# Optimization experiments

Measured on AMD Instinct MI355X. Metric: run time of the kernel, lower is better.

## Reference

```python
import jax, jax.numpy as jnp
import numpy as np

B, S, D_IN, D_OUT, H = 4, 2048, 1024, 1024, 16
HD = D_OUT // H  # head_dim = 64


def setup_inputs() -> dict:
    key = jax.random.key(0)
    ks = jax.random.split(key, 7)
    sd_in = 1.0 / np.sqrt(D_IN)
    sd_out = 1.0 / np.sqrt(D_OUT)
    return {
        "x": jax.random.normal(ks[0], (B, S, D_IN), dtype=jnp.float32),
        # weights stored [in, out] so y = x @ W (equivalent to torch Linear)
        "wq": jax.random.uniform(ks[1], (D_IN, D_OUT), jnp.float32, -sd_in, sd_in),
        "wk": jax.random.uniform(ks[2], (D_IN, D_OUT), jnp.float32, -sd_in, sd_in),
        "wv": jax.random.uniform(ks[3], (D_IN, D_OUT), jnp.float32, -sd_in, sd_in),
        "wo": jax.random.uniform(ks[4], (D_OUT, D_OUT), jnp.float32, -sd_out, sd_out),
        "bo": jax.random.uniform(ks[5], (D_OUT,), jnp.float32, -sd_out, sd_out),
    }


def reference(x, wq, wk, wv, wo, bo):
    b, n, _ = x.shape
    # project and split heads: [b, h, n, hd]
    q = (x @ wq).reshape(b, n, H, HD).transpose(0, 2, 1, 3)
    k = (x @ wk).reshape(b, n, H, HD).transpose(0, 2, 1, 3)
    v = (x @ wv).reshape(b, n, H, HD).transpose(0, 2, 1, 3)
    scale = 1.0 / jnp.sqrt(jnp.asarray(HD, dtype=x.dtype))
    scores = jnp.einsum('bhqd,bhkd->bhqk', q, k) * scale  # [b,h,n,n]
    causal = jnp.tril(jnp.ones((n, n), dtype=bool))
    scores = jnp.where(causal, scores, -jnp.inf)
    attn = jax.nn.softmax(scores, axis=-1)
    # dropout p=0.0 -> identity
    ctx = jnp.einsum('bhqk,bhkd->bhqd', attn, v)
    ctx = ctx.transpose(0, 2, 1, 3).reshape(b, n, D_OUT)
    return ctx @ wo + bo
```

## Files before the change

kernel.cpp:

```cpp
#include <hip/hip_runtime.h>

#define DEVINL __device__ __forceinline__

typedef __attribute__((ext_vector_type(8))) short s8v;
typedef __attribute__((ext_vector_type(4))) float f4v;
typedef __attribute__((ext_vector_type(16))) float f16v;
typedef __attribute__((ext_vector_type(8))) __bf16 bf8v;
typedef __attribute__((ext_vector_type(4))) unsigned int u4v;

static constexpr int SEQ = 2048;
static constexpr int DIM = 1024;
static constexpr int NH = 16;

DEVINL unsigned short f2bf(float f) {
  unsigned int u = __builtin_bit_cast(unsigned int, f);
  u += 0x7FFFu + ((u >> 16) & 1u);
  return (unsigned short)(u >> 16);
}

DEVINL void gl_lds16(const void* g, void* l) {
  __builtin_amdgcn_global_load_lds((__attribute__((address_space(1))) void*)g,
                                   (__attribute__((address_space(3))) void*)l,
                                   16, 0, 0);
}

DEVINL f4v mfma16(s8v a, s8v b, f4v c) {
  return __builtin_amdgcn_mfma_f32_16x16x32_bf16(__builtin_bit_cast(bf8v, a),
                                                 __builtin_bit_cast(bf8v, b),
                                                 c, 0, 0, 0);
}

DEVINL f16v mfma32(s8v a, s8v b, f16v c) {
  return __builtin_amdgcn_mfma_f32_32x32x16_bf16(__builtin_bit_cast(bf8v, a),
                                                 __builtin_bit_cast(bf8v, b),
                                                 c, 0, 0, 0);
}

DEVINL unsigned cvtpk(float lo, float hi) {
  unsigned r;
  asm("v_cvt_pk_bf16_f32 %0, %1, %2" : "=v"(r) : "v"(lo), "v"(hi));
  return r;
}

DEVINL void plswap(unsigned& a, unsigned& b) {
#if __has_builtin(__builtin_amdgcn_permlane32_swap)
  typedef int i2v __attribute__((ext_vector_type(2)));
  i2v r = __builtin_amdgcn_permlane32_swap((int)a, (int)b, false, false);
  a = (unsigned)r[0]; b = (unsigned)r[1];
#else
  asm volatile("v_permlane32_swap_b32 %0, %1" : "+v"(a), "+v"(b));
#endif
}

DEVINL s8v mkfrag(unsigned w0, unsigned w1, unsigned w2, unsigned w3) {
  u4v t = {w0, w1, w2, w3};
  return __builtin_bit_cast(s8v, t);
}

__global__ __launch_bounds__(256) void k_cvt(const float* __restrict__ in,
                                             unsigned short* __restrict__ outp) {
  const int i = blockIdx.x * 256 + threadIdx.x;
  const f4v* p = (const f4v*)in + (size_t)i * 2;
  f4v a = p[0], b = p[1];
  s8v o;
  o[0] = (short)f2bf(a[0]); o[1] = (short)f2bf(a[1]);
  o[2] = (short)f2bf(a[2]); o[3] = (short)f2bf(a[3]);
  o[4] = (short)f2bf(b[0]); o[5] = (short)f2bf(b[1]);
  o[6] = (short)f2bf(b[2]); o[7] = (short)f2bf(b[3]);
  ((s8v*)outp)[i] = o;
}

__global__ __launch_bounds__(256) void k_twt(const float* __restrict__ w0, const float* __restrict__ w1,
                                             const float* __restrict__ w2, const float* __restrict__ w3,
                                             unsigned short* __restrict__ o0, unsigned short* __restrict__ o1,
                                             unsigned short* __restrict__ o2, unsigned short* __restrict__ o3) {
  __shared__ float tile[32][33];
  const float* w = blockIdx.z == 0 ? w0 : blockIdx.z == 1 ? w1 : blockIdx.z == 2 ? w2 : w3;
  unsigned short* o = blockIdx.z == 0 ? o0 : blockIdx.z == 1 ? o1 : blockIdx.z == 2 ? o2 : o3;
  const int r0 = blockIdx.y * 32, c0 = blockIdx.x * 32;
  const int tx = threadIdx.x & 31, ty = threadIdx.x >> 5;
#pragma unroll
  for (int i = 0; i < 32; i += 8) tile[ty + i][tx] = w[(r0 + ty + i) * DIM + c0 + tx];
  __syncthreads();
#pragma unroll
  for (int i = 0; i < 32; i += 8) o[(c0 + ty + i) * DIM + r0 + tx] = f2bf(tile[tx][ty + i]);
}

static constexpr int SLOT = 49152;
static constexpr int RING_LDS = 147456;

DEVINL void stage_ab(const unsigned short* __restrict__ A, const unsigned short* __restrict__ Bt,
                     int m0, int n0, int k0, char* slot, int tid) {
#pragma unroll
  for (int ld = 0; ld < 2; ++ld) {
    const int c = ld * 512 + tid;
    const int row = c >> 3;
    const int csw = ((c & 7) ^ (row & 7)) * 8;
    gl_lds16(A + (size_t)(m0 + row) * 1024 + k0 + csw, slot + c * 16);
  }
#pragma unroll
  for (int ld = 0; ld < 4; ++ld) {
    const int c = ld * 512 + tid;
    const int row = c >> 3;
    const int csw = ((c & 7) ^ (row & 7)) * 8;
    gl_lds16(Bt + (size_t)(n0 + row) * 1024 + k0 + csw, slot + 16384 + c * 16);
  }
}

DEVINL void gemm_ring3(const unsigned short* __restrict__ A, const unsigned short* __restrict__ Bt,
                       int m0, int n0, char* smem, f4v acc[4][4]) {
  const int tid = threadIdx.x;
  const int lane = tid & 63, l15 = lane & 15, lg = lane >> 4;
  const int wid = tid >> 6, wm = wid >> 2, wn = wid & 3;
  constexpr int NT = 16;

  stage_ab(A, Bt, m0, n0, 0, smem, tid);
  stage_ab(A, Bt, m0, n0, 64, smem + SLOT, tid);

  for (int t = 0; t < NT; ++t) {
    if (t + 2 < NT) {
      stage_ab(A, Bt, m0, n0, (t + 2) * 64, smem + ((t + 2) % 3) * SLOT, tid);
      asm volatile("s_waitcnt vmcnt(12)" ::: "memory");
    } else if (t + 2 == NT) {
      asm volatile("s_waitcnt vmcnt(6)" ::: "memory");
    } else {
      asm volatile("s_waitcnt vmcnt(0)" ::: "memory");
    }
    __builtin_amdgcn_s_barrier();
    __builtin_amdgcn_sched_barrier(0);

    char* Ar = smem + (t % 3) * SLOT;
    char* Br = Ar + 16384;
#pragma unroll
    for (int kk = 0; kk < 2; ++kk) {
      s8v af[4];
#pragma unroll
      for (int mf = 0; mf < 4; ++mf) {
        const int row = wm * 64 + mf * 16 + l15;
        af[mf] = *(const s8v*)(Ar + row * 128 + ((kk * 64 + lg * 16) ^ ((row & 7) << 4)));
      }
#pragma unroll
      for (int nh = 0; nh < 2; ++nh) {
        s8v bfr[2];
#pragma unroll
        for (int j = 0; j < 2; ++j) {
          const int row = wn * 64 + (nh * 2 + j) * 16 + l15;
          bfr[j] = *(const s8v*)(Br + row * 128 + ((kk * 64 + lg * 16) ^ ((row & 7) << 4)));
        }
        __builtin_amdgcn_s_setprio(1);
#pragma unroll
        for (int mf = 0; mf < 4; ++mf) {
          acc[mf][nh * 2 + 0] = mfma16(af[mf], bfr[0], acc[mf][nh * 2 + 0]);
          acc[mf][nh * 2 + 1] = mfma16(af[mf], bfr[1], acc[mf][nh * 2 + 1]);
        }
        __builtin_amdgcn_s_setprio(0);
      }
    }
    __builtin_amdgcn_sched_barrier(0);
    __builtin_amdgcn_s_barrier();
  }
}

__global__ __launch_bounds__(512, 2) void k_qkv(const unsigned short* __restrict__ xb,
                                                const unsigned short* __restrict__ wqt,
                                                const unsigned short* __restrict__ wkt,
                                                const unsigned short* __restrict__ wvt,
                                                unsigned short* __restrict__ q,
                                                unsigned short* __restrict__ k,
                                                unsigned short* __restrict__ v) {
  extern __shared__ __align__(16) char smem[];
  const int wgid = (blockIdx.x & 7) * 96 + (blockIdx.x >> 3);
  const int m0 = (wgid / 12) * 128;
  const int rem = wgid % 12;
  const int which = rem >> 2;
  const int n0 = (rem & 3) * 256;
  const unsigned short* Bt = which == 0 ? wqt : which == 1 ? wkt : wvt;
  unsigned short* C = which == 0 ? q : which == 1 ? k : v;
  const float oscale = which == 0 ? 0.125f * 1.44269504f : 1.0f;
  f4v acc[4][4];
  const f4v z = {0.f, 0.f, 0.f, 0.f};
#pragma unroll
  for (int a = 0; a < 4; ++a)
#pragma unroll
    for (int b = 0; b < 4; ++b) acc[a][b] = z;
  gemm_ring3(xb, Bt, m0, n0, smem, acc);
  const int lane = threadIdx.x & 63, l15 = lane & 15, lg = lane >> 4;
  const int wid = threadIdx.x >> 6, wm = wid >> 2, wn = wid & 3;
#pragma unroll
  for (int mf = 0; mf < 4; ++mf)
#pragma unroll
    for (int nf = 0; nf < 4; ++nf)
#pragma unroll
      for (int r = 0; r < 4; ++r) {
        const int row = m0 + wm * 64 + mf * 16 + lg * 4 + r;
        const int col = n0 + wn * 64 + nf * 16 + l15;
        C[(size_t)row * 1024 + col] = f2bf(acc[mf][nf][r] * oscale);
      }
}

__global__ __launch_bounds__(512, 2) void k_oproj(const unsigned short* __restrict__ ctx,
                                                  const unsigned short* __restrict__ wot,
                                                  const float* __restrict__ bo,
                                                  float* __restrict__ outp) {
  extern __shared__ __align__(16) char smem[];
  const int wgid = (blockIdx.x & 7) * 32 + (blockIdx.x >> 3);
  const int m0 = (wgid >> 2) * 128;
  const int n0 = (wgid & 3) * 256;
  f4v acc[4][4];
  const f4v z = {0.f, 0.f, 0.f, 0.f};
#pragma unroll
  for (int a = 0; a < 4; ++a)
#pragma unroll
    for (int b = 0; b < 4; ++b) acc[a][b] = z;
  gemm_ring3(ctx, wot, m0, n0, smem, acc);
  const int lane = threadIdx.x & 63, l15 = lane & 15, lg = lane >> 4;
  const int wid = threadIdx.x >> 6, wm = wid >> 2, wn = wid & 3;
#pragma unroll
  for (int nf = 0; nf < 4; ++nf) {
    const int col = n0 + wn * 64 + nf * 16 + l15;
    const float bias = bo[col];
#pragma unroll
    for (int mf = 0; mf < 4; ++mf)
#pragma unroll
      for (int r = 0; r < 4; ++r) {
        const int row = m0 + wm * 64 + mf * 16 + lg * 4 + r;
        outp[(size_t)row * 1024 + col] = acc[mf][nf][r] + bias;
      }
  }
}

__global__ __launch_bounds__(256) void k_tv(const unsigned short* __restrict__ v,
                                            unsigned short* __restrict__ vt) {
  __shared__ unsigned short tile[64][65];
  const int b = blockIdx.z, h = blockIdx.y, s0 = blockIdx.x * 64;
  const int t = threadIdx.x;
#pragma unroll
  for (int i = 0; i < 16; ++i) {
    const int s = i * 4 + (t >> 6), d = t & 63;
    tile[s][d] = v[(size_t)(b * SEQ + s0 + s) * 1024 + h * 64 + d];
  }
  __syncthreads();
#pragma unroll
  for (int i = 0; i < 16; ++i) {
    const int d = i * 4 + (t >> 6), s = t & 63;
    vt[(size_t)((b * NH + h) * 64 + d) * SEQ + s0 + s] = tile[s][d];
  }
}

DEVINL void stage_kv(const unsigned short* __restrict__ kbase,
                     const unsigned short* __restrict__ vbase,
                     int kv0, char* Ks, char* Vs, int tid) {
#pragma unroll
  for (int i = 0; i < 2; ++i) {
    const int c = i * 256 + tid;
    const int row = c >> 3;
    const int csw = ((c & 7) ^ (row & 7)) * 8;
    gl_lds16(kbase + (size_t)(kv0 + row) * 1024 + csw, Ks + c * 16);
    gl_lds16(vbase + (size_t)row * SEQ + kv0 + csw, Vs + c * 16);
  }
}

__global__ __launch_bounds__(256) void k_attn(const unsigned short* __restrict__ q,
                                              const unsigned short* __restrict__ kg,
                                              const unsigned short* __restrict__ vt,
                                              unsigned short* __restrict__ ctx) {
  __shared__ __align__(16) char smem[32768];
  const int b = blockIdx.z, h = blockIdx.y, pair = blockIdx.x;
  const int tid = threadIdx.x, lane = tid & 63, w = tid >> 6;
  const int l31 = lane & 31, hi = lane >> 5;

  const unsigned short* kbase = kg + (size_t)b * SEQ * 1024 + h * 64;
  const unsigned short* vbase = vt + (size_t)((b * NH + h) * 64) * SEQ;

  f16v z16;
#pragma unroll
  for (int i = 0; i < 16; ++i) z16[i] = 0.f;

  for (int seg = 0; seg < 2; ++seg) {
    const int qi = seg == 0 ? pair : 15 - pair;
    const int qbb = qi * 128;
    const int qg = qbb + w * 32 + l31;
    const unsigned short* qp = q + (size_t)(b * SEQ + qg) * 1024 + h * 64;
    s8v qf[4];
#pragma unroll
    for (int kd = 0; kd < 4; ++kd) qf[kd] = *(const s8v*)(qp + kd * 16 + hi * 8);

    f16v o0 = z16, o1 = z16;
    float m = -3e38f, lsum = 0.f;
    const int nt = qi * 2 + 2;

    __syncthreads();
    stage_kv(kbase, vbase, 0, smem, smem + 16384, tid);

    for (int t = 0; t < nt; ++t) {
      const int kv0 = t * 64;
      char* Ks = smem + (t & 1) * 8192;
      char* Vs = smem + 16384 + (t & 1) * 8192;
      __syncthreads();
      if (t + 1 < nt)
        stage_kv(kbase, vbase, kv0 + 64, smem + ((t + 1) & 1) * 8192,
                 smem + 16384 + ((t + 1) & 1) * 8192, tid);
      if (kv0 > qbb + w * 32 + 31) continue;

      f16v s0 = z16, s1 = z16;
#pragma unroll
      for (int kd = 0; kd < 4; ++kd) {
        const int off = kd * 32 + hi * 16;
        const int r0 = l31, r1 = 32 + l31;
        const s8v kf0 = *(const s8v*)(Ks + r0 * 128 + (off ^ ((r0 & 7) << 4)));
        const s8v kf1 = *(const s8v*)(Ks + r1 * 128 + (off ^ ((r1 & 7) << 4)));
        s0 = mfma32(kf0, qf[kd], s0);
        s1 = mfma32(kf1, qf[kd], s1);
      }

      const bool needmask = (kv0 + 63 > qbb + w * 32);
      const int crel = qg - kv0;
      float tmax = -3e38f;
#pragma unroll
      for (int r = 0; r < 16; ++r) {
        const int kvloc = (r & 3) + 8 * (r >> 2) + 4 * hi;
        float v0 = s0[r], v1 = s1[r];
        if (needmask) {
          if (kvloc > crel) v0 = -3e38f;
          if (kvloc + 32 > crel) v1 = -3e38f;
        }
        s0[r] = v0; s1[r] = v1;
        tmax = fmaxf(tmax, fmaxf(v0, v1));
      }
      tmax = fmaxf(tmax, __shfl_xor(tmax, 32));

      const bool grew = tmax > m + 8.f;
      const float mnew = grew ? tmax : m;
      const float corr = __builtin_amdgcn_exp2f(m - mnew);
      m = mnew;

      float rs = 0.f;
#pragma unroll
      for (int r = 0; r < 16; ++r) {
        const float e0 = __builtin_amdgcn_exp2f(s0[r] - m);
        const float e1 = __builtin_amdgcn_exp2f(s1[r] - m);
        s0[r] = e0; s1[r] = e1;
        rs += e0 + e1;
      }
      rs += __shfl_xor(rs, 32);
      lsum = lsum * corr + rs;
      if (__any(grew)) { o0 *= corr; o1 *= corr; }

      unsigned a0 = cvtpk(s0[0], s0[1]), b0 = cvtpk(s0[4], s0[5]); plswap(a0, b0);
      unsigned a1 = cvtpk(s0[2], s0[3]), b1 = cvtpk(s0[6], s0[7]); plswap(a1, b1);
      const s8v f0 = mkfrag(a0, a1, b0, b1);
      unsigned a2 = cvtpk(s0[8], s0[9]), b2 = cvtpk(s0[12], s0[13]); plswap(a2, b2);
      unsigned a3 = cvtpk(s0[10], s0[11]), b3 = cvtpk(s0[14], s0[15]); plswap(a3, b3);
      const s8v f1 = mkfrag(a2, a3, b2, b3);
      unsigned a4 = cvtpk(s1[0], s1[1]), b4 = cvtpk(s1[4], s1[5]); plswap(a4, b4);
      unsigned a5 = cvtpk(s1[2], s1[3]), b5 = cvtpk(s1[6], s1[7]); plswap(a5, b5);
      const s8v f2 = mkfrag(a4, a5, b4, b5);
      unsigned a6 = cvtpk(s1[8], s1[9]), b6 = cvtpk(s1[12], s1[13]); plswap(a6, b6);
      unsigned a7 = cvtpk(s1[10], s1[11]), b7 = cvtpk(s1[14], s1[15]); plswap(a7, b7);
      const s8v f3 = mkfrag(a6, a7, b6, b7);

#pragma unroll
      for (int ks = 0; ks < 4; ++ks) {
        const s8v pb = ks == 0 ? f0 : ks == 1 ? f1 : ks == 2 ? f2 : f3;
        const int off = ks * 32 + hi * 16;
        const int rd0 = l31, rd1 = 32 + l31;
        const s8v v0 = *(const s8v*)(Vs + rd0 * 128 + (off ^ ((rd0 & 7) << 4)));
        const s8v v1 = *(const s8v*)(Vs + rd1 * 128 + (off ^ ((rd1 & 7) << 4)));
        o0 = mfma32(v0, pb, o0);
        o1 = mfma32(v1, pb, o1);
      }
    }

    const float rl = 1.f / lsum;
    unsigned short* crow_p = ctx + (size_t)(b * SEQ + qg) * 1024 + h * 64;
#pragma unroll
    for (int r = 0; r < 16; ++r) {
      const int d = (r & 3) + 8 * (r >> 2) + 4 * hi;
      crow_p[d] = f2bf(o0[r] * rl);
      crow_p[32 + d] = f2bf(o1[r] * rl);
    }
  }
}

extern "C" void kernel_launch(void* const* d_in, const int* in_sizes, int n_in,
                              void* d_out, int out_size, void* d_ws, size_t ws_size,
                              hipStream_t stream) {
  (void)in_sizes; (void)n_in; (void)out_size; (void)ws_size;
  const float* x = (const float*)d_in[0];
  const float* wq = (const float*)d_in[1];
  const float* wk = (const float*)d_in[2];
  const float* wv = (const float*)d_in[3];
  const float* wo = (const float*)d_in[4];
  const float* bo = (const float*)d_in[5];
  float* outp = (float*)d_out;
  char* ws = (char*)d_ws;
  const size_t MB = 1ull << 20;
  unsigned short* xb  = (unsigned short*)(ws + 0 * MB);
  unsigned short* wqt = (unsigned short*)(ws + 16 * MB);
  unsigned short* wkt = (unsigned short*)(ws + 18 * MB);
  unsigned short* wvt = (unsigned short*)(ws + 20 * MB);
  unsigned short* wot = (unsigned short*)(ws + 22 * MB);
  unsigned short* qb_ = (unsigned short*)(ws + 24 * MB);
  unsigned short* kb_ = (unsigned short*)(ws + 40 * MB);
  unsigned short* vb_ = (unsigned short*)(ws + 56 * MB);
  unsigned short* vtb = (unsigned short*)(ws + 72 * MB);
  unsigned short* ctx = (unsigned short*)(ws + 88 * MB);

  (void)hipFuncSetAttribute((const void*)k_qkv, hipFuncAttributeMaxDynamicSharedMemorySize, RING_LDS);
  (void)hipFuncSetAttribute((const void*)k_oproj, hipFuncAttributeMaxDynamicSharedMemorySize, RING_LDS);

  k_cvt<<<4096, 256, 0, stream>>>(x, xb);
  k_twt<<<dim3(32, 32, 4), 256, 0, stream>>>(wq, wk, wv, wo, wqt, wkt, wvt, wot);
  k_qkv<<<768, 512, RING_LDS, stream>>>(xb, wqt, wkt, wvt, qb_, kb_, vb_);
  k_tv<<<dim3(32, 16, 4), 256, 0, stream>>>(vb_, vtb);
  k_attn<<<dim3(8, 16, 4), 256, 0, stream>>>(qb_, kb_, vtb, ctx);
  k_oproj<<<256, 512, RING_LDS, stream>>>(ctx, wot, bo, outp);
}
```

Measured before the change: 258.9 us.

## Split attention into one block per query tile and retile output projection

The attention kernel stops pairing a short and a long causal query tile in one block and launches one block per 128-row query tile, doubling the grid to 1024 blocks. Each block now has uneven work, so balance relies on the hardware scheduler rather than the pairing. The output projection switches from 512-thread 128x256 tiles on a 3-stage ring to 256-thread 128x128 tiles on a new 2-stage double-buffered pipeline in static LDS with 512 blocks. This gives more blocks for occupancy and tail coverage, at the cost of shallower prefetch and more redundant loads per output.

Result: slower. 305.8 us (+18.1%).

```diff
diff --git a/kernel.cpp b/kernel.cpp
--- a/kernel.cpp
+++ b/kernel.cpp
@@ -198,23 +198,86 @@
       }
 }
 
-__global__ __launch_bounds__(512, 2) void k_oproj(const unsigned short* __restrict__ ctx,
-                                                  const unsigned short* __restrict__ wot,
-                                                  const float* __restrict__ bo,
-                                                  float* __restrict__ outp) {
-  extern __shared__ __align__(16) char smem[];
-  const int wgid = (blockIdx.x & 7) * 32 + (blockIdx.x >> 3);
-  const int m0 = (wgid >> 2) * 128;
-  const int n0 = (wgid & 3) * 256;
+DEVINL void stage128(const unsigned short* __restrict__ A, const unsigned short* __restrict__ Bt,
+                     int m0, int n0, int k0, char* Ab, char* Bb, int tid) {
+#pragma unroll
+  for (int ld = 0; ld < 4; ++ld) {
+    const int c = ld * 256 + tid;
+    const int row = c >> 3;
+    const int csw = ((c & 7) ^ (row & 7)) * 8;
+    gl_lds16(A + (size_t)(m0 + row) * 1024 + k0 + csw, Ab + c * 16);
+    gl_lds16(Bt + (size_t)(n0 + row) * 1024 + k0 + csw, Bb + c * 16);
+  }
+}
+
+DEVINL void gemm_compute_tile(char* Ar, char* Br, f4v acc[4][4],
+                              int l15, int lg, int wm, int wn) {
+#pragma unroll
+  for (int kk = 0; kk < 2; ++kk) {
+    s8v af[4], bfr[4];
+    const int kb2 = (kk * 32 + lg * 8) * 2;
+#pragma unroll
+    for (int mf = 0; mf < 4; ++mf) {
+      const int row = wm * 64 + mf * 16 + l15;
+      af[mf] = *(const s8v*)(Ar + row * 128 + (kb2 ^ ((row & 7) << 4)));
+    }
+#pragma unroll
+    for (int nf = 0; nf < 4; ++nf) {
+      const int row = wn * 64 + nf * 16 + l15;
+      bfr[nf] = *(const s8v*)(Br + row * 128 + (kb2 ^ ((row & 7) << 4)));
+    }
+#pragma unroll
+    for (int mf = 0; mf < 4; ++mf)
+#pragma unroll
+      for (int nf = 0; nf < 4; ++nf) acc[mf][nf] = mfma16(af[mf], bfr[nf], acc[mf][nf]);
+  }
+}
+
+DEVINL void gemm_ring2(const unsigned short* __restrict__ A, const unsigned short* __restrict__ Bt,
+                       int m0, int n0, char* smem, f4v acc[4][4]) {
+  const int tid = threadIdx.x;
+  const int lane = tid & 63, l15 = lane & 15, lg = lane >> 4;
+  const int wm = (tid >> 6) >> 1, wn = (tid >> 6) & 1;
+  constexpr int NT = 16;
+
+  stage128(A, Bt, m0, n0, 0, smem, smem + 32768, tid);
+
+  for (int t = 0; t < NT - 1; ++t) {
+    const int nb = (t + 1) & 1;
+    stage128(A, Bt, m0, n0, (t + 1) * 64, smem + nb * 16384, smem + 32768 + nb * 16384, tid);
+    asm volatile("s_waitcnt vmcnt(8)" ::: "memory");
+    __builtin_amdgcn_s_barrier();
+    __builtin_amdgcn_sched_barrier(0);
+    const int cb = t & 1;
+    gemm_compute_tile(smem + cb * 16384, smem + 32768 + cb * 16384, acc, l15, lg, wm, wn);
+    asm volatile("s_waitcnt lgkmcnt(0)" ::: "memory");
+    __builtin_amdgcn_sched_barrier(0);
+    __builtin_amdgcn_s_barrier();
+  }
+  asm volatile("s_waitcnt vmcnt(0)" ::: "memory");
+  __builtin_amdgcn_s_barrier();
+  __builtin_amdgcn_sched_barrier(0);
+  gemm_compute_tile(smem + ((NT - 1) & 1) * 16384, smem + 32768 + ((NT - 1) & 1) * 16384,
+                    acc, l15, lg, wm, wn);
+}
+
+__global__ __launch_bounds__(256) void k_oproj(const unsigned short* __restrict__ ctx,
+                                               const unsigned short* __restrict__ wot,
+                                               const float* __restrict__ bo,
+                                               float* __restrict__ outp) {
+  __shared__ __align__(16) char smem[65536];
+  const int wgid = (blockIdx.x & 7) * 64 + (blockIdx.x >> 3);
+  const int m0 = (wgid >> 3) * 128;
+  const int n0 = (wgid & 7) * 128;
   f4v acc[4][4];
   const f4v z = {0.f, 0.f, 0.f, 0.f};
 #pragma unroll
   for (int a = 0; a < 4; ++a)
 #pragma unroll
     for (int b = 0; b < 4; ++b) acc[a][b] = z;
-  gemm_ring3(ctx, wot, m0, n0, smem, acc);
+  gemm_ring2(ctx, wot, m0, n0, smem, acc);
   const int lane = threadIdx.x & 63, l15 = lane & 15, lg = lane >> 4;
-  const int wid = threadIdx.x >> 6, wm = wid >> 2, wn = wid & 3;
+  const int wm = (threadIdx.x >> 6) >> 1, wn = (threadIdx.x >> 6) & 1;
 #pragma unroll
   for (int nf = 0; nf < 4; ++nf) {
     const int col = n0 + wn * 64 + nf * 16 + l15;
@@ -265,7 +328,7 @@
                                               const unsigned short* __restrict__ vt,
                                               unsigned short* __restrict__ ctx) {
   __shared__ __align__(16) char smem[32768];
-  const int b = blockIdx.z, h = blockIdx.y, pair = blockIdx.x;
+  const int b = blockIdx.z, h = blockIdx.y, qi = blockIdx.x;
   const int tid = threadIdx.x, lane = tid & 63, w = tid >> 6;
   const int l31 = lane & 31, hi = lane >> 5;
 
@@ -276,109 +339,105 @@
 #pragma unroll
   for (int i = 0; i < 16; ++i) z16[i] = 0.f;
 
-  for (int seg = 0; seg < 2; ++seg) {
-    const int qi = seg == 0 ? pair : 15 - pair;
-    const int qbb = qi * 128;
-    const int qg = qbb + w * 32 + l31;
-    const unsigned short* qp = q + (size_t)(b * SEQ + qg) * 1024 + h * 64;
-    s8v qf[4];
-#pragma unroll
-    for (int kd = 0; kd < 4; ++kd) qf[kd] = *(const s8v*)(qp + kd * 16 + hi * 8);
-
-    f16v o0 = z16, o1 = z16;
-    float m = -3e38f, lsum = 0.f;
-    const int nt = qi * 2 + 2;
-
+  const int qbb = qi * 128;
+  const int qg = qbb + w * 32 + l31;
+  const unsigned short* qp = q + (size_t)(b * SEQ + qg) * 1024 + h * 64;
+  s8v qf[4];
+#pragma unroll
+  for (int kd = 0; kd < 4; ++kd) qf[kd] = *(const s8v*)(qp + kd * 16 + hi * 8);
+
+  f16v o0 = z16, o1 = z16;
+  float m = -3e38f, lsum = 0.f;
+  const int nt = qi * 2 + 2;
+
+  stage_kv(kbase, vbase, 0, smem, smem + 16384, tid);
+
+  for (int t = 0; t < nt; ++t) {
+    const int kv0 = t * 64;
+    char* Ks = smem + (t & 1) * 8192;
+    char* Vs = smem + 16384 + (t & 1) * 8192;
     __syncthreads();
-    stage_kv(kbase, vbase, 0, smem, smem + 16384, tid);
-
-    for (int t = 0; t < nt; ++t) {
-      const int kv0 = t * 64;
-      char* Ks = smem + (t & 1) * 8192;
-      char* Vs = smem + 16384 + (t & 1) * 8192;
-      __syncthreads();
-      if (t + 1 < nt)
-        stage_kv(kbase, vbase, kv0 + 64, smem + ((t + 1) & 1) * 8192,
-                 smem + 16384 + ((t + 1) & 1) * 8192, tid);
-      if (kv0 > qbb + w * 32 + 31) continue;
-
-      f16v s0 = z16, s1 = z16;
-#pragma unroll
-      for (int kd = 0; kd < 4; ++kd) {
-        const int off = kd * 32 + hi * 16;
-        const int r0 = l31, r1 = 32 + l31;
-        const s8v kf0 = *(const s8v*)(Ks + r0 * 128 + (off ^ ((r0 & 7) << 4)));
-        const s8v kf1 = *(const s8v*)(Ks + r1 * 128 + (off ^ ((r1 & 7) << 4)));
-        s0 = mfma32(kf0, qf[kd], s0);
-        s1 = mfma32(kf1, qf[kd], s1);
+    if (t + 1 < nt)
+      stage_kv(kbase, vbase, kv0 + 64, smem + ((t + 1) & 1) * 8192,
+               smem + 16384 + ((t + 1) & 1) * 8192, tid);
+    if (kv0 > qbb + w * 32 + 31) continue;
+
+    f16v s0 = z16, s1 = z16;
+#pragma unroll
+    for (int kd = 0; kd < 4; ++kd) {
+      const int off = kd * 32 + hi * 16;
+      const int r0 = l31, r1 = 32 + l31;
+      const s8v kf0 = *(const s8v*)(Ks + r0 * 128 + (off ^ ((r0 & 7) << 4)));
+      const s8v kf1 = *(const s8v*)(Ks + r1 * 128 + (off ^ ((r1 & 7) << 4)));
+      s0 = mfma32(kf0, qf[kd], s0);
+      s1 = mfma32(kf1, qf[kd], s1);
+    }
+
+    const bool needmask = (kv0 + 63 > qbb + w * 32);
+    const int crel = qg - kv0;
+    float tmax = -3e38f;
+#pragma unroll
+    for (int r = 0; r < 16; ++r) {
+      const int kvloc = (r & 3) + 8 * (r >> 2) + 4 * hi;
+      float v0 = s0[r], v1 = s1[r];
+      if (needmask) {
+        if (kvloc > crel) v0 = -3e38f;
+        if (kvloc + 32 > crel) v1 = -3e38f;
       }
-
-      const bool needmask = (kv0 + 63 > qbb + w * 32);
-      const int crel = qg - kv0;
-      float tmax = -3e38f;
-#pragma unroll
-      for (int r = 0; r < 16; ++r) {
-        const int kvloc = (r & 3) + 8 * (r >> 2) + 4 * hi;
-        float v0 = s0[r], v1 = s1[r];
-        if (needmask) {
-          if (kvloc > crel) v0 = -3e38f;
-          if (kvloc + 32 > crel) v1 = -3e38f;
-        }
-        s0[r] = v0; s1[r] = v1;
-        tmax = fmaxf(tmax, fmaxf(v0, v1));
-      }
-      tmax = fmaxf(tmax, __shfl_xor(tmax, 32));
-
-      const bool grew = tmax > m + 8.f;
-      const float mnew = grew ? tmax : m;
-      const float corr = __builtin_amdgcn_exp2f(m - mnew);
-      m = mnew;
-
-      float rs = 0.f;
-#pragma unroll
-      for (int r = 0; r < 16; ++r) {
-        const float e0 = __builtin_amdgcn_exp2f(s0[r] - m);
-        const float e1 = __builtin_amdgcn_exp2f(s1[r] - m);
-        s0[r] = e0; s1[r] = e1;
-        rs += e0 + e1;
-      }
-      rs += __shfl_xor(rs, 32);
-      lsum = lsum * corr + rs;
-      if (__any(grew)) { o0 *= corr; o1 *= corr; }
-
-      unsigned a0 = cvtpk(s0[0], s0[1]), b0 = cvtpk(s0[4], s0[5]); plswap(a0, b0);
-      unsigned a1 = cvtpk(s0[2], s0[3]), b1 = cvtpk(s0[6], s0[7]); plswap(a1, b1);
-      const s8v f0 = mkfrag(a0, a1, b0, b1);
-      unsigned a2 = cvtpk(s0[8], s0[9]), b2 = cvtpk(s0[12], s0[13]); plswap(a2, b2);
-      unsigned a3 = cvtpk(s0[10], s0[11]), b3 = cvtpk(s0[14], s0[15]); plswap(a3, b3);
-      const s8v f1 = mkfrag(a2, a3, b2, b3);
-      unsigned a4 = cvtpk(s1[0], s1[1]), b4 = cvtpk(s1[4], s1[5]); plswap(a4, b4);
-      unsigned a5 = cvtpk(s1[2], s1[3]), b5 = cvtpk(s1[6], s1[7]); plswap(a5, b5);
-      const s8v f2 = mkfrag(a4, a5, b4, b5);
-      unsigned a6 = cvtpk(s1[8], s1[9]), b6 = cvtpk(s1[12], s1[13]); plswap(a6, b6);
-      unsigned a7 = cvtpk(s1[10], s1[11]), b7 = cvtpk(s1[14], s1[15]); plswap(a7, b7);
-      const s8v f3 = mkfrag(a6, a7, b6, b7);
-
-#pragma unroll
-      for (int ks = 0; ks < 4; ++ks) {
-        const s8v pb = ks == 0 ? f0 : ks == 1 ? f1 : ks == 2 ? f2 : f3;
-        const int off = ks * 32 + hi * 16;
-        const int rd0 = l31, rd1 = 32 + l31;
-        const s8v v0 = *(const s8v*)(Vs + rd0 * 128 + (off ^ ((rd0 & 7) << 4)));
-        const s8v v1 = *(const s8v*)(Vs + rd1 * 128 + (off ^ ((rd1 & 7) << 4)));
-        o0 = mfma32(v0, pb, o0);
-        o1 = mfma32(v1, pb, o1);
-      }
-    }
-
-    const float rl = 1.f / lsum;
-    unsigned short* crow_p = ctx + (size_t)(b * SEQ + qg) * 1024 + h * 64;
+      s0[r] = v0; s1[r] = v1;
+      tmax = fmaxf(tmax, fmaxf(v0, v1));
+    }
+    tmax = fmaxf(tmax, __shfl_xor(tmax, 32));
+
+    const bool grew = tmax > m + 8.f;
+    const float mnew = grew ? tmax : m;
+    const float corr = __builtin_amdgcn_exp2f(m - mnew);
+    m = mnew;
+
+    float rs = 0.f;
 #pragma unroll
     for (int r = 0; r < 16; ++r) {
-      const int d = (r & 3) + 8 * (r >> 2) + 4 * hi;
-      crow_p[d] = f2bf(o0[r] * rl);
-      crow_p[32 + d] = f2bf(o1[r] * rl);
-    }
+      const float e0 = __builtin_amdgcn_exp2f(s0[r] - m);
+      const float e1 = __builtin_amdgcn_exp2f(s1[r] - m);
+      s0[r] = e0; s1[r] = e1;
+      rs += e0 + e1;
+    }
+    rs += __shfl_xor(rs, 32);
+    lsum = lsum * corr + rs;
+    if (__any(grew)) { o0 *= corr; o1 *= corr; }
+
+    unsigned a0 = cvtpk(s0[0], s0[1]), b0 = cvtpk(s0[4], s0[5]); plswap(a0, b0);
+    unsigned a1 = cvtpk(s0[2], s0[3]), b1 = cvtpk(s0[6], s0[7]); plswap(a1, b1);
+    const s8v f0 = mkfrag(a0, a1, b0, b1);
+    unsigned a2 = cvtpk(s0[8], s0[9]), b2 = cvtpk(s0[12], s0[13]); plswap(a2, b2);
+    unsigned a3 = cvtpk(s0[10], s0[11]), b3 = cvtpk(s0[14], s0[15]); plswap(a3, b3);
+    const s8v f1 = mkfrag(a2, a3, b2, b3);
+    unsigned a4 = cvtpk(s1[0], s1[1]), b4 = cvtpk(s1[4], s1[5]); plswap(a4, b4);
+    unsigned a5 = cvtpk(s1[2], s1[3]), b5 = cvtpk(s1[6], s1[7]); plswap(a5, b5);
+    const s8v f2 = mkfrag(a4, a5, b4, b5);
+    unsigned a6 = cvtpk(s1[8], s1[9]), b6 = cvtpk(s1[12], s1[13]); plswap(a6, b6);
+    unsigned a7 = cvtpk(s1[10], s1[11]), b7 = cvtpk(s1[14], s1[15]); plswap(a7, b7);
+    const s8v f3 = mkfrag(a6, a7, b6, b7);
+
+#pragma unroll
+    for (int ks = 0; ks < 4; ++ks) {
+      const s8v pb = ks == 0 ? f0 : ks == 1 ? f1 : ks == 2 ? f2 : f3;
+      const int off = ks * 32 + hi * 16;
+      const int rd0 = l31, rd1 = 32 + l31;
+      const s8v v0 = *(const s8v*)(Vs + rd0 * 128 + (off ^ ((rd0 & 7) << 4)));
+      const s8v v1 = *(const s8v*)(Vs + rd1 * 128 + (off ^ ((rd1 & 7) << 4)));
+      o0 = mfma32(v0, pb, o0);
+      o1 = mfma32(v1, pb, o1);
+    }
+  }
+
+  const float rl = 1.f / lsum;
+  unsigned short* crow_p = ctx + (size_t)(b * SEQ + qg) * 1024 + h * 64;
+#pragma unroll
+  for (int r = 0; r < 16; ++r) {
+    const int d = (r & 3) + 8 * (r >> 2) + 4 * hi;
+    crow_p[d] = f2bf(o0[r] * rl);
+    crow_p[32 + d] = f2bf(o1[r] * rl);
   }
 }
 
@@ -407,12 +466,11 @@
   unsigned short* ctx = (unsigned short*)(ws + 88 * MB);
 
   (void)hipFuncSetAttribute((const void*)k_qkv, hipFuncAttributeMaxDynamicSharedMemorySize, RING_LDS);
-  (void)hipFuncSetAttribute((const void*)k_oproj, hipFuncAttributeMaxDynamicSharedMemorySize, RING_LDS);
 
   k_cvt<<<4096, 256, 0, stream>>>(x, xb);
   k_twt<<<dim3(32, 32, 4), 256, 0, stream>>>(wq, wk, wv, wo, wqt, wkt, wvt, wot);
   k_qkv<<<768, 512, RING_LDS, stream>>>(xb, wqt, wkt, wvt, qb_, kb_, vb_);
   k_tv<<<dim3(32, 16, 4), 256, 0, stream>>>(vb_, vtb);
-  k_attn<<<dim3(8, 16, 4), 256, 0, stream>>>(qb_, kb_, vtb, ctx);
-  k_oproj<<<256, 512, RING_LDS, stream>>>(ctx, wot, bo, outp);
-}
+  k_attn<<<dim3(16, 16, 4), 256, 0, stream>>>(qb_, kb_, vtb, ctx);
+  k_oproj<<<512, 256, 0, stream>>>(ctx, wot, bo, outp);
+}
```
